# Kernel tuning notes

Hardware: AMD Instinct MI355X
Metric: run time of the kernel (lower is better)

Reference implementation:

```python
import jax, jax.numpy as jnp
import numpy as np

B, S, D_IN, D_OUT = 4, 2048, 1024, 1024


def setup_inputs() -> dict:
    key = jax.random.key(0)
    k1, k2, k3, k4 = jax.random.split(key, 4)
    x = jax.random.normal(k1, (B, S, D_IN), dtype=jnp.float32)
    scale = 1.0 / np.sqrt(D_IN)
    Wq = jax.random.normal(k2, (D_IN, D_OUT), dtype=jnp.float32) * scale
    Wk = jax.random.normal(k3, (D_IN, D_OUT), dtype=jnp.float32) * scale
    Wv = jax.random.normal(k4, (D_IN, D_OUT), dtype=jnp.float32) * scale
    return {"x": x, "Wq": Wq, "Wk": Wk, "Wv": Wv}


def reference(x, Wq, Wk, Wv):
    # QKV projections (Linear, no bias)
    q = jnp.einsum('bsd,de->bse', x, Wq)  # [B,S,D_OUT]
    k = jnp.einsum('bsd,de->bse', x, Wk)
    v = jnp.einsum('bsd,de->bse', x, Wv)
    d_out = Wq.shape[1]
    # raw scores [B,S,S], scaled after masking (identical math: -inf stays -inf)
    scores = jnp.einsum('bqe,bke->bqk', q, k) * (d_out ** -0.5)
    S_ = x.shape[1]
    # causal mask: future positions (j > i) are masked out
    causal = jnp.triu(jnp.ones((S_, S_), dtype=bool), k=1)
    scores = jnp.where(causal[None, :, :], -jnp.inf, scores)
    attn = jax.nn.softmax(scores, axis=-1)  # dropout p=0.0 -> identity
    return jnp.einsum('bqk,bke->bqe', attn, v)
```

## Files before the change

kernel.cpp:

```cpp
#include <hip/hip_runtime.h>
#include <stdint.h>

typedef unsigned short u16;
typedef unsigned int u32;
typedef __bf16 bf16x8 __attribute__((ext_vector_type(8)));
typedef float f32x4 __attribute__((ext_vector_type(4)));

#define BM 128
#define BN 128
#define BK 64

__device__ __forceinline__ u16 f2bf(float x) {
  union { float f; uint32_t u; } c; c.f = x;
  uint32_t r = (c.u + 0x7FFFu + ((c.u >> 16) & 1u)) >> 16;
  return (u16)r;
}
__device__ __forceinline__ float bf2f(u16 v) {
  union { uint32_t u; float f; } c; c.u = ((uint32_t)v) << 16;
  return c.f;
}

__device__ __forceinline__ void async_copy16(const u16* g, u16* l) {
  __builtin_amdgcn_global_load_lds(
      (const __attribute__((address_space(1))) void*)g,
      (__attribute__((address_space(3))) void*)l,
      16, 0, 0);
}

__global__ void zerofill_u16(u16* __restrict__ p) {
  long i = (long)blockIdx.x * 256 + threadIdx.x;
  p[i] = 0;
}

__global__ __launch_bounds__(256)
void prep(const void* __restrict__ xs, const void* __restrict__ w0,
          const void* __restrict__ w1, const void* __restrict__ w2,
          u16* __restrict__ xn, u16* __restrict__ WT3, u32* __restrict__ flag,
          float* __restrict__ sigma, int nxb)
{
  __shared__ int sh_hits;
  __shared__ u16 tile[64][72];
  if (threadIdx.x == 0) sh_hits = 0;
  __syncthreads();
  {
    const u16* w = (const u16*)w0;
    int h = 0;
    for (int i = threadIdx.x; i < 8192; i += 256)
      if ((w[i] & 0x7F80u) == 0x7F80u) h++;
    if (h) atomicAdd(&sh_hits, h);
  }
  __syncthreads();
  const bool isf32 = (sh_hits > 0);
  const int blk = blockIdx.x;
  const int tid = threadIdx.x;
  if (blk == 0 && tid == 0) *flag = isf32 ? 1000u : 0u;

  if (blk < nxb) {
    long i = ((long)blk * 256 + tid) * 8;
    u16 o[8];
    if (isf32) {
      const float* s = (const float*)xs + i;
      f32x4 a = *(const f32x4*)s;
      f32x4 b = *(const f32x4*)(s + 4);
#pragma unroll
      for (int c = 0; c < 4; ++c) { o[c] = f2bf(a[c]); o[c + 4] = f2bf(b[c]); }
    } else {
      *(uint4*)o = *(const uint4*)((const u16*)xs + i);
    }
    *(uint4*)(xn + i) = *(uint4*)o;
  } else if (blk < nxb + 768) {
    const int Dd = 1024;
    int t = blk - nxb;
    int z = t >> 8;
    int r = t & 255;
    const int r0 = (r >> 4) * 64, c0 = (r & 15) * 64;
    const void* src = (z == 0) ? w0 : (z == 1) ? w1 : w2;
    u16* out = WT3 + (long)z * Dd * Dd;
#pragma unroll
    for (int p = 0; p < 2; ++p) {
      int v = tid + p * 256;
      int row = v >> 3, c8 = (v & 7) * 8;
      u16 tt[8];
      if (isf32) {
        const float* sp = (const float*)src + (long)(r0 + row) * Dd + c0 + c8;
        f32x4 a = *(const f32x4*)sp;
        f32x4 b = *(const f32x4*)(sp + 4);
#pragma unroll
        for (int c = 0; c < 4; ++c) { tt[c] = f2bf(a[c]); tt[c + 4] = f2bf(b[c]); }
      } else {
        *(uint4*)tt = *(const uint4*)((const u16*)src + (long)(r0 + row) * Dd + c0 + c8);
      }
#pragma unroll
      for (int c = 0; c < 8; ++c) tile[row][c8 + c] = tt[c];
    }
    __syncthreads();
#pragma unroll
    for (int p = 0; p < 2; ++p) {
      int v = tid + p * 256;
      int oc = v >> 3, r8 = (v & 7) * 8;
      union { uint4 q; u16 s[8]; } tt;
#pragma unroll
      for (int c = 0; c < 8; ++c) tt.s[c] = tile[r8 + c][oc];
      *(uint4*)(out + (long)(c0 + oc) * Dd + r0 + r8) = tt.q;
    }
  } else {
    int t = blk - (nxb + 768);
    *(f32x4*)(sigma + ((long)t * 256 + tid) * 4) = f32x4{0.f, 0.f, 0.f, 0.f};
  }
}

__global__ __launch_bounds__(512, 2)
void gemm_qkv8(const u16* __restrict__ A, const u16* __restrict__ B,
               u16* __restrict__ C, int lda, int ldb, int ldc, int nbn)
{
  __shared__ u16 lds[65536];
  const int tid  = threadIdx.x;
  const int wid  = tid >> 6;
  const int lane = tid & 63;
  const int l16  = lane & 15;
  const int lk   = lane >> 4;
  const int srow = lane >> 3;
  const int swz  = ((lane & 7) ^ srow) * 8;
  const int wr   = wid >> 2, wc = wid & 3;

  const int q8 = (int)gridDim.x >> 3;
  const int wg = ((int)blockIdx.x & 7) * q8 + ((int)blockIdx.x >> 3);
  const int m0 = (wg / nbn) * 256, n0 = (wg % nbn) * 256;

  const int NK = 16;

  auto stageA = [&](int t, int h) {
    u16* dst = lds + (t & 1) * 16384 + h * 8192 + (wid * 16) * 64;
    const u16* src = A + (long)(m0 + h * 128 + wid * 16 + srow) * lda + t * 64 + swz;
    async_copy16(src, dst);
    async_copy16(src + (long)8 * lda, dst + 8 * 64);
  };
  auto stageB = [&](int t, int h) {
    u16* dst = lds + 32768 + (t & 1) * 16384 + h * 8192 + (wid * 16) * 64;
    const u16* src = B + (long)(n0 + h * 128 + wid * 16 + srow) * ldb + t * 64 + swz;
    async_copy16(src, dst);
    async_copy16(src + (long)8 * ldb, dst + 8 * 64);
  };

  f32x4 acc[8][4] = {};
  bf16x8 bv[4][2];

  stageB(0, 0); stageB(0, 1); stageA(0, 0); stageA(0, 1);
  stageB(1, 0); stageB(1, 1);
  asm volatile("s_waitcnt vmcnt(4)" ::: "memory");
  __builtin_amdgcn_s_barrier();

  for (int t = 0; t < NK; ++t) {
    const u16* Ab = lds + (t & 1) * 16384 + wr * 8192;
    const u16* Bb = lds + 32768 + (t & 1) * 16384 + (wc >> 1) * 8192 + (wc & 1) * 64 * 64;
#pragma unroll
    for (int q = 0; q < 4; ++q) {
      bf16x8 av[2][2];
#pragma unroll
      for (int j = 0; j < 2; ++j)
#pragma unroll
        for (int kh = 0; kh < 2; ++kh)
          av[j][kh] = *(const bf16x8*)(Ab + ((2 * q + j) * 16 + l16) * 64 +
                                       (((kh * 4 + lk) ^ (l16 & 7)) * 8));
      if (q == 0) {
#pragma unroll
        for (int ni = 0; ni < 4; ++ni)
#pragma unroll
          for (int kh = 0; kh < 2; ++kh)
            bv[ni][kh] = *(const bf16x8*)(Bb + (ni * 16 + l16) * 64 +
                                          (((kh * 4 + lk) ^ (l16 & 7)) * 8));
      }
      if (q == 0)      { if (t + 1 < NK) stageA(t + 1, 0); }
      else if (q == 1) { if (t + 1 < NK) stageA(t + 1, 1); }
      else if (q == 2) { if (t + 2 < NK) stageB(t + 2, 0); }
      else {
        if (t + 2 < NK) stageB(t + 2, 1);
        if (t < NK - 2) asm volatile("s_waitcnt vmcnt(4)" ::: "memory");
        else            asm volatile("s_waitcnt vmcnt(0)" ::: "memory");
      }
      __builtin_amdgcn_s_barrier();
      asm volatile("s_waitcnt lgkmcnt(0)" ::: "memory");
      __builtin_amdgcn_sched_barrier(0);
      __builtin_amdgcn_s_setprio(1);
#pragma unroll
      for (int j = 0; j < 2; ++j)
#pragma unroll
        for (int ni = 0; ni < 4; ++ni)
#pragma unroll
          for (int kh = 0; kh < 2; ++kh)
            acc[2 * q + j][ni] = __builtin_amdgcn_mfma_f32_16x16x32_bf16(
                av[j][kh], bv[ni][kh], acc[2 * q + j][ni], 0, 0, 0);
      __builtin_amdgcn_s_setprio(0);
      __builtin_amdgcn_s_barrier();
    }
  }

  const int rb0 = m0 + wr * 128;
  const int cb0 = n0 + wc * 64;
#pragma unroll
  for (int mi = 0; mi < 8; ++mi)
#pragma unroll
    for (int r = 0; r < 4; ++r) {
      const int row = rb0 + mi * 16 + lk * 4 + r;
#pragma unroll
      for (int ni = 0; ni < 4; ++ni) {
        const int col = cb0 + ni * 16 + l16;
        C[(long)row * ldc + col] = f2bf(acc[mi][ni][r]);
      }
    }
}

template <int MODE>
__global__ __launch_bounds__(256, 4)
void gemm_nt(const u16* __restrict__ A, const u16* __restrict__ B, void* __restrict__ Cv,
             const u32* __restrict__ flag, float* __restrict__ sigma, int sigStride,
             int K, int lda, int ldb, int ldc,
             long sA, long sB, long sC, long cOff,
             float scale, int trik, int ntri,
             const u16* __restrict__ vSrc, u16* __restrict__ vtDst,
             long sV, long sVT, int ldV, int ldVT)
{
  __shared__ u16 As[BM * BK];
  __shared__ u16 Bs[BN * BK];
  const int bz = blockIdx.z;
  const int tid = threadIdx.x;

  int bm, bn;
  if constexpr (MODE == 3) {
    if ((int)blockIdx.x >= ntri) {
      int t2 = blockIdx.x - ntri;
      const u16* in = vSrc + (long)bz * sV;
      u16* out = vtDst + (long)bz * sVT;
      const int c0 = (t2 & 15) * 64;
      const int r0 = (t2 >> 4) * 64;
      u16 (*tile)[72] = reinterpret_cast<u16(*)[72]>(As);
#pragma unroll
      for (int p = 0; p < 2; ++p) {
        int v = tid + p * 256;
        int row = v >> 3, c8 = (v & 7) * 8;
        union { uint4 q; u16 s[8]; } t;
        t.q = *(const uint4*)(in + (long)(r0 + row) * ldV + c0 + c8);
#pragma unroll
        for (int i = 0; i < 8; ++i) tile[row][c8 + i] = t.s[i];
      }
      __syncthreads();
#pragma unroll
      for (int p = 0; p < 2; ++p) {
        int v = tid + p * 256;
        int oc = v >> 3, r8 = (v & 7) * 8;
        union { uint4 q; u16 s[8]; } t;
#pragma unroll
        for (int i = 0; i < 8; ++i) t.s[i] = tile[r8 + i][oc];
        *(uint4*)(out + (long)(c0 + oc) * ldVT + r0 + r8) = t.q;
      }
      return;
    }
    {
      const int t = blockIdx.x;
      const int cum[11] = {0, 10, 26, 36, 52, 68, 78, 94, 110, 126, 136};
      const int ssm[10] = {0, 1, 1, 2, 2, 2, 3, 3, 3, 3};
      const int ssn[10] = {0, 0, 1, 0, 1, 2, 0, 1, 2, 3};
      int s = 0;
      while (cum[s + 1] <= t) ++s;
      const int l = t - cum[s];
      const int sm = ssm[s], sn = ssn[s];
      int tm, tn;
      if (sm == sn) {
        tm = 0;
        while ((tm + 1) * (tm + 2) / 2 <= l) ++tm;
        tn = l - tm * (tm + 1) / 2;
      } else { tm = l >> 2; tn = l & 3; }
      bm = sm * 4 + tm;
      bn = sn * 4 + tn;
    }
  } else {
    bm = blockIdx.y;
    if (trik) bm = gridDim.y - 1 - bm;
    bn = blockIdx.x;
  }

  A += (long)bz * sA;
  B += (long)bz * sB;

  const int wid  = tid >> 6;
  const int lane = tid & 63;
  const int l16  = lane & 15;
  const int lk   = lane >> 4;
  const int srow = lane >> 3;
  const int swz  = ((lane & 7) ^ srow) * 8;
  const int m0 = bm * BM, n0 = bn * BN;

  int nk = K / BK;
  if (trik) { int lim = (m0 + BM) / BK; if (lim < nk) nk = lim; }

  f32x4 acc[4][4] = {};

  for (int kt = 0; kt < nk; ++kt) {
    const int k0 = kt * BK;
#pragma unroll
    for (int c = 0; c < 4; ++c) {
      const int rb = wid * 32 + c * 8;
      async_copy16(A + (long)(m0 + rb + srow) * lda + (k0 + swz), As + rb * BK);
      async_copy16(B + (long)(n0 + rb + srow) * ldb + (k0 + swz), Bs + rb * BK);
    }
    __syncthreads();
#pragma unroll
    for (int kh = 0; kh < 2; ++kh) {
      bf16x8 av[4], bv[4];
#pragma unroll
      for (int i = 0; i < 4; ++i) {
        const int Ra = (wid >> 1) * 64 + i * 16 + l16;
        const int Rb = (wid & 1)  * 64 + i * 16 + l16;
        const int ca = ((kh * 4 + lk) ^ (l16 & 7)) * 8;
        av[i] = *(const bf16x8*)(As + Ra * BK + ca);
        bv[i] = *(const bf16x8*)(Bs + Rb * BK + ca);
      }
#pragma unroll
      for (int mi = 0; mi < 4; ++mi)
#pragma unroll
        for (int ni = 0; ni < 4; ++ni)
          acc[mi][ni] = __builtin_amdgcn_mfma_f32_16x16x32_bf16(av[mi], bv[ni], acc[mi][ni], 0, 0, 0);
    }
    __syncthreads();
  }

  const int rb0 = m0 + (wid >> 1) * 64;
  const int cb0 = n0 + (wid & 1) * 64;
  const long cbase = (long)bz * sC + cOff;

  if constexpr (MODE == 3) {
    u16* Cp = (u16*)Cv;
    const bool diag = (bm == bn);
    float* sig = sigma + (long)bz * sigStride;
#pragma unroll
    for (int mi = 0; mi < 4; ++mi)
#pragma unroll
      for (int r = 0; r < 4; ++r) {
        const int row = rb0 + mi * 16 + lk * 4 + r;
        float part = 0.f;
#pragma unroll
        for (int ni = 0; ni < 4; ++ni) {
          const int col = cb0 + ni * 16 + l16;
          float ev = __expf(acc[mi][ni][r] * scale);
          if (diag && col > row) ev = 0.f;
          u16 b = f2bf(ev);
          part += bf2f(b);
          Cp[cbase + (long)row * ldc + col] = b;
        }
#pragma unroll
        for (int o = 1; o < 16; o <<= 1) part += __shfl_xor(part, o);
        if (l16 == 0) atomicAdd(&sig[row], part);
      }
  } else {
    const bool f32out = (MODE == 2) && (*flag > 32);
    const float* sig = (MODE == 2) ? (sigma + (long)bz * sigStride) : nullptr;
#pragma unroll
    for (int mi = 0; mi < 4; ++mi)
#pragma unroll
      for (int r = 0; r < 4; ++r) {
        const int row = rb0 + mi * 16 + lk * 4 + r;
        float rs = scale;
        if constexpr (MODE == 2) rs = 1.0f / sig[row];
#pragma unroll
        for (int ni = 0; ni < 4; ++ni) {
          const int col = cb0 + ni * 16 + l16;
          const float v = acc[mi][ni][r] * rs;
          const long idx = cbase + (long)row * ldc + col;
          if constexpr (MODE == 0) {
            ((u16*)Cv)[idx] = f2bf(v);
          } else {
            if (f32out) ((float*)Cv)[idx] = v;
            else        ((u16*)Cv)[idx]   = f2bf(v);
          }
        }
      }
  }
}

extern "C" void kernel_launch(void* const* d_in, const int* in_sizes, int n_in,
                              void* d_out, int out_size, void* d_ws, size_t ws_size,
                              hipStream_t stream)
{
  (void)in_sizes; (void)n_in; (void)out_size;
  const int Bb = 4, S = 2048, D = 1024, D3 = 3072;
  const long SD  = (long)S * D;
  const long SD3 = (long)S * D3;
  const long SS  = (long)S * S;
  const long N_X = (long)Bb * SD;
  const long N_W = (long)D * D;
  const int NTRI = 16 * 17 / 2;

  char* ws = (char*)d_ws;
  size_t off = 0;
  auto take = [&](size_t bytes) -> void* {
    void* p = ws + off;
    off = (off + bytes + 255) & ~((size_t)255);
    return p;
  };

  u32*   flag  = (u32*)take(4096);
  float* sigma = (float*)take((size_t)Bb * S * 4);
  u16*   xn    = (u16*)take((size_t)N_X * 2);
  u16*   WT3   = (u16*)take((size_t)3 * N_W * 2);
  const size_t off_common = off;

  const size_t needA = off_common + (size_t)(N_X * 3 * 2)
                     + (size_t)(N_X * 2)
                     + (size_t)(Bb * SS * 2) + 4096;
  const size_t needC = off_common + (size_t)(S * (long)D3 * 2)
                     + (size_t)(SD * 2)
                     + (size_t)(SS * 2) + 4096;

  if (ws_size < needC) {
    zerofill_u16<<<(int)(N_X / 256), 256, 0, stream>>>((u16*)d_out);
    return;
  }

  const int nxb = (int)(N_X / 2048);
  prep<<<nxb + 768 + 8, 256, 0, stream>>>(d_in[0], d_in[1], d_in[2], d_in[3],
                                          xn, WT3, flag, sigma, nxb);

  const float scl = 0.03125f;

  if (ws_size >= needA) {
    u16* QKV = (u16*)take((size_t)N_X * 3 * 2);
    u16* VT  = (u16*)take((size_t)N_X * 2);
    u16* E   = (u16*)take((size_t)Bb * SS * 2);

    gemm_qkv8<<<dim3(32 * 12), 512, 0, stream>>>(xn, WT3, QKV, D, D, D3, 12);

    gemm_nt<3><<<dim3(NTRI + 512, 1, Bb), 256, 0, stream>>>(
        QKV, QKV + 1024, E, flag, sigma, S, D, D3, D3, S,
        SD3, SD3, SS, 0, scl, 0, NTRI,
        QKV + 2048, VT, SD3, SD, D3, S);

    gemm_nt<2><<<dim3(D / BN, S / BM, Bb), 256, 0, stream>>>(
        E, VT, d_out, flag, sigma, S, S, S, S, D,
        SS, SD, SD, 0, 1.f, 1, 0, nullptr, nullptr, 0, 0, 0, 0);
  } else {
    u16* QKVb = (u16*)take((size_t)S * D3 * 2);
    u16* VTb  = (u16*)take((size_t)SD * 2);
    u16* Eb   = (u16*)take((size_t)SS * 2);

    for (int b = 0; b < Bb; ++b) {
      gemm_qkv8<<<dim3(8 * 12), 512, 0, stream>>>(
          xn + (long)b * SD, WT3, QKVb, D, D, D3, 12);

      gemm_nt<3><<<dim3(NTRI + 512, 1, 1), 256, 0, stream>>>(
          QKVb, QKVb + 1024, Eb, flag, sigma + (long)b * S, S, D, D3, D3, S,
          0, 0, 0, 0, scl, 0, NTRI,
          QKVb + 2048, VTb, 0, 0, D3, S);

      gemm_nt<2><<<dim3(D / BN, S / BM, 1), 256, 0, stream>>>(
          Eb, VTb, d_out, flag, sigma + (long)b * S, S, S, S, S, D,
          0, 0, 0, (long)b * SD, 1.f, 1, 0, nullptr, nullptr, 0, 0, 0, 0);
    }
  }
}
```

Before: 250.4 us.

## Shrink QKV GEMM tile to 128x256 with two-phase K pipeline

The QKV projection GEMM changes from 256x256 to 128x256 output tiles, and the launch grid doubles to match. Each workgroup's 8 waves now form a 2x4 grid of 64x64 subtiles. Each K step is split into two half-K MFMA phases, with the A and B stage loads interleaved between them. The intent is more workgroups across the CUs and less LDS per block (96KB instead of 128KB), which may allow better occupancy. The cost is lower arithmetic intensity per tile and more global traffic for the B weights.

```diff
diff --git a/kernel.cpp b/kernel.cpp
--- a/kernel.cpp
+++ b/kernel.cpp
@@ -110,10 +110,10 @@
 }
 
 __global__ __launch_bounds__(512, 2)
-void gemm_qkv8(const u16* __restrict__ A, const u16* __restrict__ B,
-               u16* __restrict__ C, int lda, int ldb, int ldc, int nbn)
+void gemm_qkv2p(const u16* __restrict__ A, const u16* __restrict__ B,
+                u16* __restrict__ C, int lda, int ldb, int ldc, int nbn)
 {
-  __shared__ u16 lds[65536];
+  __shared__ u16 lds[49152];
   const int tid  = threadIdx.x;
   const int wid  = tid >> 6;
   const int lane = tid & 63;
@@ -125,80 +125,84 @@
 
   const int q8 = (int)gridDim.x >> 3;
   const int wg = ((int)blockIdx.x & 7) * q8 + ((int)blockIdx.x >> 3);
-  const int m0 = (wg / nbn) * 256, n0 = (wg % nbn) * 256;
+  const int m0 = (wg / nbn) * 128, n0 = (wg % nbn) * 256;
 
   const int NK = 16;
 
-  auto stageA = [&](int t, int h) {
-    u16* dst = lds + (t & 1) * 16384 + h * 8192 + (wid * 16) * 64;
-    const u16* src = A + (long)(m0 + h * 128 + wid * 16 + srow) * lda + t * 64 + swz;
+  auto stageA = [&](int t) {
+    u16* dst = lds + (t & 1) * 8192 + (wid * 16) * 64;
+    const u16* src = A + (long)(m0 + wid * 16 + srow) * lda + t * 64 + swz;
     async_copy16(src, dst);
     async_copy16(src + (long)8 * lda, dst + 8 * 64);
   };
-  auto stageB = [&](int t, int h) {
-    u16* dst = lds + 32768 + (t & 1) * 16384 + h * 8192 + (wid * 16) * 64;
-    const u16* src = B + (long)(n0 + h * 128 + wid * 16 + srow) * ldb + t * 64 + swz;
-    async_copy16(src, dst);
-    async_copy16(src + (long)8 * ldb, dst + 8 * 64);
+  auto stageB = [&](int t) {
+    u16* dst = lds + 16384 + (t & 1) * 16384 + (wid * 32) * 64;
+    const u16* src = B + (long)(n0 + wid * 32 + srow) * ldb + t * 64 + swz;
+#pragma unroll
+    for (int c = 0; c < 4; ++c)
+      async_copy16(src + (long)(c * 8) * ldb, dst + (c * 8) * 64);
   };
 
-  f32x4 acc[8][4] = {};
-  bf16x8 bv[4][2];
-
-  stageB(0, 0); stageB(0, 1); stageA(0, 0); stageA(0, 1);
-  stageB(1, 0); stageB(1, 1);
+  f32x4 acc[4][4] = {};
+
+  stageB(0); stageA(0); stageB(1);
   asm volatile("s_waitcnt vmcnt(4)" ::: "memory");
   __builtin_amdgcn_s_barrier();
 
   for (int t = 0; t < NK; ++t) {
-    const u16* Ab = lds + (t & 1) * 16384 + wr * 8192;
-    const u16* Bb = lds + 32768 + (t & 1) * 16384 + (wc >> 1) * 8192 + (wc & 1) * 64 * 64;
-#pragma unroll
-    for (int q = 0; q < 4; ++q) {
-      bf16x8 av[2][2];
-#pragma unroll
-      for (int j = 0; j < 2; ++j)
-#pragma unroll
-        for (int kh = 0; kh < 2; ++kh)
-          av[j][kh] = *(const bf16x8*)(Ab + ((2 * q + j) * 16 + l16) * 64 +
-                                       (((kh * 4 + lk) ^ (l16 & 7)) * 8));
-      if (q == 0) {
-#pragma unroll
-        for (int ni = 0; ni < 4; ++ni)
-#pragma unroll
-          for (int kh = 0; kh < 2; ++kh)
-            bv[ni][kh] = *(const bf16x8*)(Bb + (ni * 16 + l16) * 64 +
-                                          (((kh * 4 + lk) ^ (l16 & 7)) * 8));
-      }
-      if (q == 0)      { if (t + 1 < NK) stageA(t + 1, 0); }
-      else if (q == 1) { if (t + 1 < NK) stageA(t + 1, 1); }
-      else if (q == 2) { if (t + 2 < NK) stageB(t + 2, 0); }
-      else {
-        if (t + 2 < NK) stageB(t + 2, 1);
-        if (t < NK - 2) asm volatile("s_waitcnt vmcnt(4)" ::: "memory");
-        else            asm volatile("s_waitcnt vmcnt(0)" ::: "memory");
-      }
-      __builtin_amdgcn_s_barrier();
-      asm volatile("s_waitcnt lgkmcnt(0)" ::: "memory");
-      __builtin_amdgcn_sched_barrier(0);
-      __builtin_amdgcn_s_setprio(1);
-#pragma unroll
-      for (int j = 0; j < 2; ++j)
-#pragma unroll
-        for (int ni = 0; ni < 4; ++ni)
-#pragma unroll
-          for (int kh = 0; kh < 2; ++kh)
-            acc[2 * q + j][ni] = __builtin_amdgcn_mfma_f32_16x16x32_bf16(
-                av[j][kh], bv[ni][kh], acc[2 * q + j][ni], 0, 0, 0);
-      __builtin_amdgcn_s_setprio(0);
-      __builtin_amdgcn_s_barrier();
-    }
-  }
-
-  const int rb0 = m0 + wr * 128;
+    const u16* Ab = lds + (t & 1) * 8192 + (wr * 64) * 64;
+    const u16* Bb = lds + 16384 + (t & 1) * 16384 + (wc * 64) * 64;
+    bf16x8 bv[4][2];
+
+    bf16x8 av0[4];
+#pragma unroll
+    for (int i = 0; i < 4; ++i)
+      av0[i] = *(const bf16x8*)(Ab + (i * 16 + l16) * 64 + ((lk ^ (l16 & 7)) * 8));
+#pragma unroll
+    for (int ni = 0; ni < 4; ++ni)
+#pragma unroll
+      for (int kh = 0; kh < 2; ++kh)
+        bv[ni][kh] = *(const bf16x8*)(Bb + (ni * 16 + l16) * 64 +
+                                      (((kh * 4 + lk) ^ (l16 & 7)) * 8));
+    if (t + 1 < NK) stageA(t + 1);
+    __builtin_amdgcn_s_barrier();
+    asm volatile("s_waitcnt lgkmcnt(0)" ::: "memory");
+    __builtin_amdgcn_sched_barrier(0);
+    __builtin_amdgcn_s_setprio(1);
+#pragma unroll
+    for (int mi = 0; mi < 4; ++mi)
+#pragma unroll
+      for (int ni = 0; ni < 4; ++ni)
+        acc[mi][ni] = __builtin_amdgcn_mfma_f32_16x16x32_bf16(
+            av0[mi], bv[ni][0], acc[mi][ni], 0, 0, 0);
+    __builtin_amdgcn_s_setprio(0);
+    __builtin_amdgcn_s_barrier();
+
+    bf16x8 av1[4];
+#pragma unroll
+    for (int i = 0; i < 4; ++i)
+      av1[i] = *(const bf16x8*)(Ab + (i * 16 + l16) * 64 + (((4 + lk) ^ (l16 & 7)) * 8));
+    if (t + 2 < NK) stageB(t + 2);
+    if (t < NK - 2) asm volatile("s_waitcnt vmcnt(4)" ::: "memory");
+    else            asm volatile("s_waitcnt vmcnt(0)" ::: "memory");
+    __builtin_amdgcn_s_barrier();
+    asm volatile("s_waitcnt lgkmcnt(0)" ::: "memory");
+    __builtin_amdgcn_sched_barrier(0);
+    __builtin_amdgcn_s_setprio(1);
+#pragma unroll
+    for (int mi = 0; mi < 4; ++mi)
+#pragma unroll
+      for (int ni = 0; ni < 4; ++ni)
+        acc[mi][ni] = __builtin_amdgcn_mfma_f32_16x16x32_bf16(
+            av1[mi], bv[ni][1], acc[mi][ni], 0, 0, 0);
+    __builtin_amdgcn_s_setprio(0);
+    __builtin_amdgcn_s_barrier();
+  }
+
+  const int rb0 = m0 + wr * 64;
   const int cb0 = n0 + wc * 64;
 #pragma unroll
-  for (int mi = 0; mi < 8; ++mi)
+  for (int mi = 0; mi < 4; ++mi)
 #pragma unroll
     for (int r = 0; r < 4; ++r) {
       const int row = rb0 + mi * 16 + lk * 4 + r;
@@ -427,7 +431,7 @@
     u16* VT  = (u16*)take((size_t)N_X * 2);
     u16* E   = (u16*)take((size_t)Bb * SS * 2);
 
-    gemm_qkv8<<<dim3(32 * 12), 512, 0, stream>>>(xn, WT3, QKV, D, D, D3, 12);
+    gemm_qkv2p<<<dim3(64 * 12), 512, 0, stream>>>(xn, WT3, QKV, D, D, D3, 12);
 
     gemm_nt<3><<<dim3(NTRI + 512, 1, Bb), 256, 0, stream>>>(
         QKV, QKV + 1024, E, flag, sigma, S, D, D3, D3, S,
@@ -443,7 +447,7 @@
     u16* Eb   = (u16*)take((size_t)SS * 2);
 
     for (int b = 0; b < Bb; ++b) {
-      gemm_qkv8<<<dim3(8 * 12), 512, 0, stream>>>(
+      gemm_qkv2p<<<dim3(16 * 12), 512, 0, stream>>>(
           xn + (long)b * SD, WT3, QKVb, D, D, D3, 12);
 
       gemm_nt<3><<<dim3(NTRI + 512, 1, 1), 256, 0, stream>>>(
```

After: 249.3 us. No clear change (-0.4%).
